# Kernel optimization log

Measured on AMD Instinct MI355X. Metric: run time of the kernel, lower is better.

The kernel has to match this reference:

```python
import jax, jax.numpy as jnp
import numpy as np
from jax import lax

V = 9; C1 = 80; C2 = 40; C4 = 24; CH = 32
H1, W1 = 30, 40; H2, W2 = 60, 80; H4, W4 = 120, 160
SHAPE = (96, 96, 96); N = 131072; EPS = 1e-5
OFFS = np.stack(np.meshgrid(np.arange(-1, 2), np.arange(-1, 2), np.arange(-1, 2), indexing='ij'), -1).reshape(-1, 3).astype(np.int32)  # 27 kernel offsets


def conv2d(x, w, b):
    y = lax.conv_general_dilated(x, w, (1, 1), 'SAME', dimension_numbers=('NCHW', 'OIHW', 'NCHW'))
    return y + b[None, :, None, None]


def bn1d(x, g, b):  # eval-mode BatchNorm1d (running_mean=0, running_var=1)
    return g * x * (1.0 / np.sqrt(1.0 + EPS)) + b


def layernorm(x, g, b):
    m = x.mean(-1, keepdims=True)
    v = ((x - m) ** 2).mean(-1, keepdims=True)
    return (x - m) / jnp.sqrt(v + EPS) * g + b


def grid_sample_zeros(img, gx, gy):
    # img [V,C,H,W]; gx,gy [V,M] normalized to [-1,1]; bilinear, align_corners=True, zeros padding
    Vn, C, H, W = img.shape
    px = (gx + 1.0) * 0.5 * (W - 1)
    py = (gy + 1.0) * 0.5 * (H - 1)
    x0 = jnp.floor(px); y0 = jnp.floor(py)
    wx = px - x0; wy = py - y0
    flat = img.reshape(Vn, C, H * W)
    def corner(xc, yc, wgt):
        valid = (xc >= 0) & (xc <= W - 1) & (yc >= 0) & (yc <= H - 1)
        xi = jnp.clip(xc, 0, W - 1).astype(jnp.int32)
        yi = jnp.clip(yc, 0, H - 1).astype(jnp.int32)
        idx = yi * W + xi  # [V,M]
        g = jax.vmap(lambda f, i: f[:, i])(flat, idx)  # [V,C,M]
        return g * (wgt * valid)[:, None, :]
    return (corner(x0, y0, (1 - wx) * (1 - wy)) + corner(x0 + 1, y0, wx * (1 - wy))
            + corner(x0, y0 + 1, (1 - wx) * wy) + corner(x0 + 1, y0 + 1, wx * wy))


def subm_conv(feat, W3, cxyz, grid):
    # submanifold sparse 3x3x3 conv: per-offset gather of active neighbors -> GEMM -> accumulate
    n = feat.shape[0]
    shp = jnp.asarray(SHAPE, jnp.int32)
    out = jnp.zeros((n, W3.shape[-1]), feat.dtype)
    for k in range(27):
        nc = cxyz + jnp.asarray(OFFS[k])
        inb = jnp.all((nc >= 0) & (nc < shp), axis=1)
        ncc = jnp.clip(nc, 0, shp - 1)
        idx = grid[ncc[:, 0], ncc[:, 1], ncc[:, 2]]
        ok = (inb & (idx >= 0)).astype(feat.dtype)
        g = feat[jnp.clip(idx, 0, n - 1)] * ok[:, None]
        out = out + g @ W3[k]
    return out


def _forward(feats_1x, feats_2x, feats_4x, origin, voxel_size, KRcam,
             w_f1, b_f1, w_f2, b_f2, w_f4, b_f4, w_down, b_down,
             w_p1, b_p1, w_p2, b_p2, w_p3, b_p3, w_p4, b_p4,
             bn0_g, bn0_b, w_elan, w_s1, ln1_g, ln1_b, w_s2, ln2_g, ln2_b,
             w_s3, ln3_g, ln3_b, w_s4, bn4_g, bn4_b,
             coords, stage, min_view_number):
    # feat_fusion_pre (bs=1, take batch 0)
    f1 = jax.nn.relu(conv2d(feats_1x[:, 0], w_f1, b_f1))
    f2 = jax.nn.relu(conv2d(feats_2x[:, 0], w_f2, b_f2))
    f4 = jax.nn.relu(conv2d(feats_4x[:, 0], w_f4, b_f4))
    f1 = jax.image.resize(f1, (V, C1, H2, W2), 'bilinear')  # F.interpolate x2
    f4 = f4.reshape(V, C4, H2, 2, W2, 2).mean(axis=(3, 5))  # AvgPool2d(2)
    fuse = jnp.concatenate([f1, f2, f4], axis=1)
    fuse = jax.nn.relu(conv2d(fuse, w_down, b_down))
    for w, b in ((w_p1, b_p1), (w_p2, b_p2), (w_p3, b_p3), (w_p4, b_p4)):
        fuse = fuse + jax.nn.relu(conv2d(fuse, w, b))  # residual blocks -> [V,CH,H2,W2]
    # multi-view projection
    cxyz = coords[:, 1:]
    world = cxyz.astype(jnp.float32) * voxel_size + origin[0]
    hom = jnp.concatenate([world, jnp.ones_like(world[:, :1])], axis=1)  # [N,4]
    im_p = jnp.einsum('vij,nj->vin', KRcam[:, 0], hom)  # [V,3,N]
    im_z = im_p[:, 2]
    gx = 2.0 * (im_p[:, 0] / im_z) / (W4 - 1) - 1.0
    gy = 2.0 * (im_p[:, 1] / im_z) / (H4 - 1) - 1.0
    mask = (jnp.abs(gx) <= 1) & (jnp.abs(gy) <= 1) & (im_z > 0)  # [V,N]
    count = mask.sum(0).astype(jnp.float32)
    # inputs are constructed so every voxel is seen by all views: valid_voxel compaction == identity
    feats = grid_sample_zeros(fuse, gx, gy) * mask[:, None, :]  # [V,CH,N]
    feat = feats.transpose(2, 0, 1)  # [N,V,CH]
    m = mask.T.astype(feat.dtype)  # [N,V]
    den = m.sum(1, keepdims=True)
    mean = (m[..., None] * feat).sum(1) / den
    var = (m[..., None] * (feat - mean[:, None, :]) ** 2).sum(1) / den  # [N,CH]
    # sparse subm conv chain
    sc = cxyz // (2 ** (2 - stage))  # stage=2 -> identity
    grid = jnp.full(SHAPE, -1, jnp.int32).at[sc[:, 0], sc[:, 1], sc[:, 2]].set(jnp.arange(N, dtype=jnp.int32))
    x = bn1d(var, bn0_g, bn0_b)
    x = jax.nn.relu(subm_conv(x, w_elan, sc, grid))  # Spares3dELAN stand-in
    r = jax.nn.relu(subm_conv(x, w_s1, sc, grid)); x = layernorm(r + x, ln1_g, ln1_b)
    r = jax.nn.relu(subm_conv(x, w_s2, sc, grid)); x = layernorm(r + x, ln2_g, ln2_b)
    r = jax.nn.relu(subm_conv(x, w_s3, sc, grid)); x = layernorm(r + x, ln3_g, ln3_b)
    occ = bn1d(subm_conv(x, w_s4, sc, grid), bn4_g, bn4_b)  # [N,1]
    return occ, coords, count


def setup_inputs() -> dict:
    key = jax.random.key(0)
    keys = jax.random.split(key, 40)
    ki = iter(range(40))
    def rn(shape, s=1.0):
        return jax.random.normal(keys[next(ki)], shape, jnp.float32) * s
    inp = {}
    inp['feats_1x'] = rn((V, 1, C1, H1, W1))
    inp['feats_2x'] = rn((V, 1, C2, H2, W2))
    inp['feats_4x'] = rn((V, 1, C4, H4, W4))
    flat = np.arange(N, dtype=np.int64) * 6  # unique active voxels in a 96^3 grid
    cx = flat // (96 * 96); rem = flat % (96 * 96)
    inp['coords'] = jnp.asarray(np.stack([np.zeros(N, np.int64), cx, rem // 96, rem % 96], 1), jnp.int32)
    inp['origin'] = jnp.asarray([[-1.92, -1.92, 1.0]], jnp.float32)
    inp['voxel_size'] = jnp.float32(0.04)
    fx, fy = 38.0, 28.0
    P = np.zeros((V, 1, 3, 4), np.float32)
    for v in range(V):
        P[v, 0] = np.array([[fx, 0.0, (W4 - 1) / 2, fx * 0.02 * (v - 4)],
                            [0.0, fy, (H4 - 1) / 2, 0.0],
                            [0.0, 0.0, 1.0, 0.0]], np.float32)
    inp['KRcam'] = jnp.asarray(P)
    s = 0.05
    inp['w_f1'] = rn((C1, C1, 3, 3), s); inp['b_f1'] = rn((C1,), s)
    inp['w_f2'] = rn((C2, C2, 3, 3), s); inp['b_f2'] = rn((C2,), s)
    inp['w_f4'] = rn((C4, C4, 3, 3), s); inp['b_f4'] = rn((C4,), s)
    inp['w_down'] = rn((CH, C1 + C2 + C4, 1, 1), s); inp['b_down'] = rn((CH,), s)
    for i in (1, 2, 3, 4):
        inp['w_p%d' % i] = rn((CH, CH, 3, 3), s); inp['b_p%d' % i] = rn((CH,), s)
    inp['bn0_g'] = jnp.ones((CH,), jnp.float32); inp['bn0_b'] = jnp.zeros((CH,), jnp.float32)
    inp['w_elan'] = rn((27, CH, CH), s)
    inp['w_s1'] = rn((27, CH, CH), s); inp['ln1_g'] = jnp.ones((CH,), jnp.float32); inp['ln1_b'] = jnp.zeros((CH,), jnp.float32)
    inp['w_s2'] = rn((27, CH, CH), s); inp['ln2_g'] = jnp.ones((CH,), jnp.float32); inp['ln2_b'] = jnp.zeros((CH,), jnp.float32)
    inp['w_s3'] = rn((27, CH, CH), s); inp['ln3_g'] = jnp.ones((CH,), jnp.float32); inp['ln3_b'] = jnp.zeros((CH,), jnp.float32)
    inp['w_s4'] = rn((27, CH, 1), s); inp['bn4_g'] = jnp.ones((1,), jnp.float32); inp['bn4_b'] = jnp.zeros((1,), jnp.float32)
    inp['stage'] = 2
    inp['min_view_number'] = 1
    return inp


def reference(feats_1x, feats_2x, feats_4x, origin, voxel_size, KRcam,
              w_f1, b_f1, w_f2, b_f2, w_f4, b_f4, w_down, b_down,
              w_p1, b_p1, w_p2, b_p2, w_p3, b_p3, w_p4, b_p4,
              bn0_g, bn0_b, w_elan, w_s1, ln1_g, ln1_b, w_s2, ln2_g, ln2_b,
              w_s3, ln3_g, ln3_b, w_s4, bn4_g, bn4_b,
              coords, stage, min_view_number):
    return _forward(feats_1x, feats_2x, feats_4x, origin, voxel_size, KRcam,
                    w_f1, b_f1, w_f2, b_f2, w_f4, b_f4, w_down, b_down,
                    w_p1, b_p1, w_p2, b_p2, w_p3, b_p3, w_p4, b_p4,
                    bn0_g, bn0_b, w_elan, w_s1, ln1_g, ln1_b, w_s2, ln2_g, ln2_b,
                    w_s3, ln3_g, ln3_b, w_s4, bn4_g, bn4_b,
                    coords, stage, min_view_number)
```

## Files before the change

### kernel.cpp

```cpp
#include <hip/hip_runtime.h>
#include <math.h>

#define VN 9
#define NVOX 131072
#define GS 96
static constexpr float INVS = 0.9999950000374997f;

typedef short bf16x8 __attribute__((ext_vector_type(8)));
typedef float f32x4v __attribute__((ext_vector_type(4)));

__device__ inline float4 ld4(const float* p){ return *reinterpret_cast<const float4*>(p); }

__device__ inline ushort f2b(float f){
  unsigned u = __float_as_uint(f);
  unsigned r = (u + 0x7fffu + ((u >> 16) & 1u)) >> 16;
  return (ushort)r;
}
__device__ inline float b2f(ushort s){ return __uint_as_float(((unsigned)s) << 16); }
__device__ inline float blo(unsigned u){ return __uint_as_float(u << 16); }
__device__ inline float bhi(unsigned u){ return __uint_as_float(u & 0xffff0000u); }

__device__ inline float4 ld4b(const ushort* p){
  uint2 u = *reinterpret_cast<const uint2*>(p);
  float4 r; r.x = blo(u.x); r.y = bhi(u.x); r.z = blo(u.y); r.w = bhi(u.y); return r;
// ... 117 lines not shown
  int wave = tid >> 6;
  int vbase = bid*(MT*64) + wave*(MT*16);
  int m = lane & 15, q = lane >> 4;
  int HW = H*W;
  int p[MT], py[MT], px[MT]; bool pin[MT];
  #pragma unroll
  for (int t = 0; t < MT; ++t){
    int pp = vbase + t*16 + m;
    pin[t] = pp < total;
    if (pp > total-1) pp = total-1;
    p[t] = pp;
    int v = pp / HW; int rem = pp - v*HW;
    int y = rem / W;
    py[t] = y; px[t] = rem - y*W;
  }
  f32x4v acc[MT][NT];
  #pragma unroll
  for (int t = 0; t < MT; ++t)
    #pragma unroll
    for (int n = 0; n < NT; ++n) acc[t][n] = 0.f;
  bf16x8 z = (short)0;

  #pragma unroll 1
  for (int tap = 0; tap < TAPS; ++tap){
    int dy = (TAPS == 9) ? tap/3 - 1 : 0;
    int dx = (TAPS == 9) ? tap%3 - 1 : 0;
    int off = dy*W + dx;
    bool val[MT];
    #pragma unroll
    for (int t = 0; t < MT; ++t)
      val[t] = pin[t] && ((unsigned)(py[t]+dy) < (unsigned)H)
                      && ((unsigned)(px[t]+dx) < (unsigned)W);
    #pragma unroll
    for (int ck = 0; ck < CK; ++ck){
      bf16x8 Af[MT], Bf[NT];
      #pragma unroll
      for (int t = 0; t < MT; ++t){
        size_t idx = val[t] ? (size_t)(p[t]+off) : 0;
        bf16x8 a = *(const bf16x8*)(fin + idx*CIN + ck*32 + q*8);
        Af[t] = val[t] ? a : z;
      }
      #pragma unroll
      for (int n = 0; n < NT; ++n)
        Bf[n] = *(const bf16x8*)(w2 + ((size_t)((tap*CK+ck)*COP + n*16 + m))*32 + q*8);
      #pragma unroll
      for (int t = 0; t < MT; ++t)
        #pragma unroll
        for (int n = 0; n < NT; ++n)
          acc[t][n] = __builtin_amdgcn_mfma_f32_16x16x32_bf16(Bf[n], Af[t], acc[t][n], 0, 0, 0);
    }
  }

  #pragma unroll
  for (int n = 0; n < NT; ++n){
    int co4 = n*16 + q*4;
    bool cok = co4 < Cout;
    float4 bs = cok ? ld4(bias + co4) : float4{0.f,0.f,0.f,0.f};
    #pragma unroll
    for (int t = 0; t < MT; ++t){
      int pp = vbase + t*16 + m;
      if (pp < total && cok){
        float4 v;
        v.x = fmaxf(acc[t][n][0] + bs.x, 0.f);
        v.y = fmaxf(acc[t][n][1] + bs.y, 0.f);
        v.z = fmaxf(acc[t][n][2] + bs.z, 0.f);
        v.w = fmaxf(acc[t][n][3] + bs.w, 0.f);
        st4b(outp + (size_t)pp*outStride + outOff + co4, v);
      }
    }
  }
}

template<int TH, int NT>
__device__ void conv_lds_dev(
    const ushort* __restrict__ fin, const ushort* __restrict__ w2,
    const float* __restrict__ bias, ushort* __restrict__ outp,
    int H, int W, int Cout, int outStride,
    const ushort* __restrict__ skipin, ushort* lds, int bid, int tid){
  constexpr int RPW = TH/4;
  constexpr int PS = 36;
  int xtiles = W >> 4;
  int ytiles = (H + TH - 1) / TH;
  int v  = bid / (ytiles*xtiles);
  int rem = bid - v*(ytiles*xtiles);
  int ty = (rem / xtiles) * TH;
  int tx = (rem % xtiles) * 16;
  const ushort* ibase = fin + (size_t)v*H*W*32;
  for (int i = tid; i < (TH+2)*18*4; i += 256){
    int chunk = i & 3;
    int pxi = i >> 2;
    int ly = pxi / 18, lx = pxi - ly*18;
    int gy = ty + ly - 1, gx = tx + lx - 1;
    uint4 d = {0,0,0,0};
    if ((unsigned)gy < (unsigned)H && (unsigned)gx < (unsigned)W)
      d = *(const uint4*)(ibase + ((size_t)gy*W + gx)*32 + chunk*8);
    *(uint4*)(lds + (size_t)(ly*18 + lx)*PS + chunk*8) = d;
  }
  __syncthreads();
  int lane = tid & 63;
  int wave = tid >> 6;
  int m = lane & 15, q = lane >> 4;
  f32x4v acc[RPW][NT];
  #pragma unroll
  for (int t = 0; t < RPW; ++t)
    #pragma unroll
    for (int n = 0; n < NT; ++n) acc[t][n] = 0.f;

  #pragma unroll 1
  for (int tap = 0; tap < 9; ++tap){
    int dy = tap/3 - 1, dx = tap%3 - 1;
    bf16x8 Af[RPW], Bf[NT];
    #pragma unroll
    for (int t = 0; t < RPW; ++t){
      int ly = wave*RPW + t + 1 + dy;
      int lx = m + 1 + dx;
      Af[t] = *(const bf16x8*)(lds + (size_t)(ly*18 + lx)*PS + q*8);
    }
    #pragma unroll
    for (int n = 0; n < NT; ++n)
      Bf[n] = *(const bf16x8*)(w2 + ((size_t)(tap*(NT*16) + n*16 + m))*32 + q*8);
    #pragma unroll
    for (int t = 0; t < RPW; ++t)
      #pragma unroll
      for (int n = 0; n < NT; ++n)
        acc[t][n] = __builtin_amdgcn_mfma_f32_16x16x32_bf16(Bf[n], Af[t], acc[t][n], 0, 0, 0);
  }

  #pragma unroll
  for (int n = 0; n < NT; ++n){
    int co4 = n*16 + q*4;
    bool cok = co4 < Cout;
    float4 bs = cok ? ld4(bias + co4) : float4{0.f,0.f,0.f,0.f};
    #pragma unroll
    for (int t = 0; t < RPW; ++t){
      int y = ty + wave*RPW + t;
      int x = tx + m;
      if (y < H && cok){
        size_t pp = (size_t)(v*H + y)*W + x;
        float4 val;
        val.x = fmaxf(acc[t][n][0] + bs.x, 0.f);
        val.y = fmaxf(acc[t][n][1] + bs.y, 0.f);
        val.z = fmaxf(acc[t][n][2] + bs.z, 0.f);
        val.w = fmaxf(acc[t][n][3] + bs.w, 0.f);
        if (skipin){
          float4 sk = ld4b(skipin + pp*32 + co4);
          val.x += sk.x; val.y += sk.y; val.z += sk.z; val.w += sk.w;
        }
        st4b(outp + pp*outStride + co4, val);
      }
    }
  }
}

__global__ __launch_bounds__(256) void k_conv_lds4(
    const ushort* __restrict__ fin, const ushort* __restrict__ w2,
    const float* __restrict__ bias, ushort* __restrict__ outp,
    const ushort* __restrict__ skipin){
  __shared__ ushort lds[6*18*36];
  conv_lds_dev<4,2>(fin, w2, bias, outp, 60, 80, 32, 32, skipin, lds, blockIdx.x, threadIdx.x);
}

__global__ __launch_bounds__(256) void k_down_p0(
    const ushort* __restrict__ fcat, const ushort* __restrict__ wdn,
    const float* __restrict__ b_dn, const ushort* __restrict__ wp0,
    const float* __restrict__ b_p0, ushort* __restrict__ outB){
  __shared__ ushort ldsA[6*18*36];
  int bid = blockIdx.x;
  int tid = threadIdx.x;
  int v  = bid / 75;
  int rem = bid - v*75;
  int ty = (rem / 5) * 4;
  int tx = (rem % 5) * 16;
  int lane = tid & 63;
  int wave = tid >> 6;
  int m = lane & 15, q = lane >> 4;
  bf16x8 z = (short)0;

  #pragma unroll
  for (int t = 0; t < 2; ++t){
    int hp = (wave*2 + t)*16 + m;
    int hpc = hp < 108 ? hp : 107;
    int ly = hpc / 18, lx = hpc - ly*18;
    int gy = ty + ly - 1, gx = tx + lx - 1;
    bool ok = (hp < 108) && ((unsigned)gy < 60u) && ((unsigned)gx < 80u);
    size_t pbase = ((size_t)(v*60 + (ok ? gy : 0))*80 + (ok ? gx : 0))*160;
    f32x4v acc0 = 0.f, acc1 = 0.f;
    #pragma unroll
    for (int ck = 0; ck < 5; ++ck){
      bf16x8 a = *(const bf16x8*)(fcat + pbase + ck*32 + q*8);
      if (!ok) a = z;
      bf16x8 w0 = *(const bf16x8*)(wdn + ((size_t)(ck*32 + m))*32 + q*8);
      bf16x8 w1 = *(const bf16x8*)(wdn + ((size_t)(ck*32 + 16 + m))*32 + q*8);
      acc0 = __builtin_amdgcn_mfma_f32_16x16x32_bf16(w0, a, acc0, 0, 0, 0);
      acc1 = __builtin_amdgcn_mfma_f32_16x16x32_bf16(w1, a, acc1, 0, 0, 0);
    }
    if (hp < 108){
      float4 bs0 = ld4(b_dn + q*4);
      float4 bs1 = ld4(b_dn + 16 + q*4);
      float4 v0, v1;
      v0.x = ok ? fmaxf(acc0[0] + bs0.x, 0.f) : 0.f;
      v0.y = ok ? fmaxf(acc0[1] + bs0.y, 0.f) : 0.f;
      v0.z = ok ? fmaxf(acc0[2] + bs0.z, 0.f) : 0.f;
      v0.w = ok ? fmaxf(acc0[3] + bs0.w, 0.f) : 0.f;
      v1.x = ok ? fmaxf(acc1[0] + bs1.x, 0.f) : 0.f;
      v1.y = ok ? fmaxf(acc1[1] + bs1.y, 0.f) : 0.f;
      v1.z = ok ? fmaxf(acc1[2] + bs1.z, 0.f) : 0.f;
      v1.w = ok ? fmaxf(acc1[3] + bs1.w, 0.f) : 0.f;
      st4b(ldsA + (size_t)(ly*18 + lx)*36 + q*4,      v0);
      st4b(ldsA + (size_t)(ly*18 + lx)*36 + 16 + q*4, v1);
    }
  }
  __syncthreads();

  f32x4v pacc0 = 0.f, pacc1 = 0.f;
  #pragma unroll 1
  for (int tap = 0; tap < 9; ++tap){
    int dy = tap/3 - 1, dx = tap%3 - 1;
    bf16x8 Af = *(const bf16x8*)(ldsA + (size_t)((wave+1+dy)*18 + (m+1+dx))*36 + q*8);
    bf16x8 B0 = *(const bf16x8*)(wp0 + ((size_t)(tap*32 + m))*32 + q*8);
    bf16x8 B1 = *(const bf16x8*)(wp0 + ((size_t)(tap*32 + 16 + m))*32 + q*8);
    pacc0 = __builtin_amdgcn_mfma_f32_16x16x32_bf16(B0, Af, pacc0, 0, 0, 0);
    pacc1 = __builtin_amdgcn_mfma_f32_16x16x32_bf16(B1, Af, pacc1, 0, 0, 0);
  }
  int y = ty + wave, x = tx + m;
  size_t pp = (size_t)(v*60 + y)*80 + x;
  #pragma unroll
  for (int n = 0; n < 2; ++n){
    int co4 = n*16 + q*4;
    float4 bs = ld4(b_p0 + co4);
    f32x4v& pa = n ? pacc1 : pacc0;
    float4 sk = ld4b(ldsA + (size_t)((wave+1)*18 + (m+1))*36 + co4);
    float4 val;
    val.x = fmaxf(pa[0] + bs.x, 0.f) + sk.x;
    val.y = fmaxf(pa[1] + bs.y, 0.f) + sk.y;
    val.z = fmaxf(pa[2] + bs.z, 0.f) + sk.z;
    val.w = fmaxf(pa[3] + bs.w, 0.f) + sk.w;
    st4b(outB + pp*32 + co4, val);
  }
}

__global__ __launch_bounds__(256) void k_p2_p3(
    const ushort* __restrict__ finA, const ushort* __restrict__ wp2,
    const float* __restrict__ b_p2, const ushort* __restrict__ wp3,
    const float* __restrict__ b_p3, ushort* __restrict__ outB){
  __shared__ ushort ldsIn[8*20*36];
  __shared__ ushort ldsMid[6*18*36];
  int bid = blockIdx.x;
  int tid = threadIdx.x;
  int v  = bid / 75;
  int rem = bid - v*75;
  int ty = (rem / 5) * 4;
  int tx = (rem % 5) * 16;
  for (int i = tid; i < 8*20*4; i += 256){
    int chunk = i & 3;
    int pxi = i >> 2;
    int ly = pxi / 20, lx = pxi - ly*20;
    int gy = ty + ly - 2, gx = tx + lx - 2;
    uint4 d = {0,0,0,0};
    if ((unsigned)gy < 60u && (unsigned)gx < 80u)
      d = *(const uint4*)(finA + ((size_t)(v*60 + gy)*80 + gx)*32 + chunk*8);
    *(uint4*)(ldsIn + (size_t)(ly*20 + lx)*36 + chunk*8) = d;
  }
  __syncthreads();
  int lane = tid & 63;
  int wave = tid >> 6;
  int m = lane & 15, q = lane >> 4;

  #pragma unroll
  for (int t = 0; t < 2; ++t){
    int hp = (wave*2 + t)*16 + m;
    int hpc = hp < 108 ? hp : 107;
    int ly = hpc / 18, lx = hpc - ly*18;
    int gy = ty + ly - 1, gx = tx + lx - 1;
    bool ok = (hp < 108) && ((unsigned)gy < 60u) && ((unsigned)gx < 80u);
    f32x4v acc0 = 0.f, acc1 = 0.f;
    #pragma unroll 1
    for (int tap = 0; tap < 9; ++tap){
      int dy = tap/3 - 1, dx = tap%3 - 1;
      bf16x8 a = *(const bf16x8*)(ldsIn + (size_t)((ly+dy+1)*20 + (lx+dx+1))*36 + q*8);
      bf16x8 w0 = *(const bf16x8*)(wp2 + ((size_t)(tap*32 + m))*32 + q*8);
      bf16x8 w1 = *(const bf16x8*)(wp2 + ((size_t)(tap*32 + 16 + m))*32 + q*8);
      acc0 = __builtin_amdgcn_mfma_f32_16x16x32_bf16(w0, a, acc0, 0, 0, 0);
      acc1 = __builtin_amdgcn_mfma_f32_16x16x32_bf16(w1, a, acc1, 0, 0, 0);
    }
    if (hp < 108){
      float4 bs0 = ld4(b_p2 + q*4);
      float4 bs1 = ld4(b_p2 + 16 + q*4);
      float4 sk0 = ld4b(ldsIn + (size_t)((ly+1)*20 + (lx+1))*36 + q*4);
      float4 sk1 = ld4b(ldsIn + (size_t)((ly+1)*20 + (lx+1))*36 + 16 + q*4);
      float4 v0, v1;
      v0.x = ok ? fmaxf(acc0[0] + bs0.x, 0.f) + sk0.x : 0.f;
      v0.y = ok ? fmaxf(acc0[1] + bs0.y, 0.f) + sk0.y : 0.f;
      v0.z = ok ? fmaxf(acc0[2] + bs0.z, 0.f) + sk0.z : 0.f;
      v0.w = ok ? fmaxf(acc0[3] + bs0.w, 0.f) + sk0.w : 0.f;
      v1.x = ok ? fmaxf(acc1[0] + bs1.x, 0.f) + sk1.x : 0.f;
      v1.y = ok ? fmaxf(acc1[1] + bs1.y, 0.f) + sk1.y : 0.f;
      v1.z = ok ? fmaxf(acc1[2] + bs1.z, 0.f) + sk1.z : 0.f;
      v1.w = ok ? fmaxf(acc1[3] + bs1.w, 0.f) + sk1.w : 0.f;
      st4b(ldsMid + (size_t)(ly*18 + lx)*36 + q*4,      v0);
      st4b(ldsMid + (size_t)(ly*18 + lx)*36 + 16 + q*4, v1);
    }
  }
  __syncthreads();

  f32x4v pacc0 = 0.f, pacc1 = 0.f;
  #pragma unroll 1
  for (int tap = 0; tap < 9; ++tap){
    int dy = tap/3 - 1, dx = tap%3 - 1;
    bf16x8 a = *(const bf16x8*)(ldsMid + (size_t)((wave+1+dy)*18 + (m+1+dx))*36 + q*8);
    bf16x8 w0 = *(const bf16x8*)(wp3 + ((size_t)(tap*32 + m))*32 + q*8);
    bf16x8 w1 = *(const bf16x8*)(wp3 + ((size_t)(tap*32 + 16 + m))*32 + q*8);
    pacc0 = __builtin_amdgcn_mfma_f32_16x16x32_bf16(w0, a, pacc0, 0, 0, 0);
    pacc1 = __builtin_amdgcn_mfma_f32_16x16x32_bf16(w1, a, pacc1, 0, 0, 0);
  }
  int y = ty + wave, x = tx + m;
  size_t pp = (size_t)(v*60 + y)*80 + x;
  #pragma unroll
  for (int n = 0; n < 2; ++n){
    int co4 = n*16 + q*4;
    float4 bs = ld4(b_p3 + co4);
    f32x4v& pa = n ? pacc1 : pacc0;
    float4 sk = ld4b(ldsMid + (size_t)((wave+1)*18 + (m+1))*36 + co4);
    float4 val;
    val.x = fmaxf(pa[0] + bs.x, 0.f) + sk.x;
    val.y = fmaxf(pa[1] + bs.y, 0.f) + sk.y;
    val.z = fmaxf(pa[2] + bs.z, 0.f) + sk.z;
    val.w = fmaxf(pa[3] + bs.w, 0.f) + sk.w;
    st4b(outB + pp*32 + co4, val);
  }
}

__device__ void scatter_dev(const int* __restrict__ coords, const int* __restrict__ stage,
                            int* __restrict__ grid, int* __restrict__ scn,
                            float* __restrict__ coords_out,
                            const float* __restrict__ origin, const float* __restrict__ vsz,
                            const float* __restrict__ KR,
                            ushort* __restrict__ sidx, float4* __restrict__ swf,
                            float* __restrict__ cnt, int n){
  int c0 = coords[n*4], c1 = coords[n*4+1], c2 = coords[n*4+2], c3 = coords[n*4+3];
  coords_out[n*4+0] = (float)c0;
  coords_out[n*4+1] = (float)c1;
  coords_out[n*4+2] = (float)c2;
  coords_out[n*4+3] = (float)c3;
  int sh = 2 - stage[0];
  int s1 = c1 >> sh, s2 = c2 >> sh, s3 = c3 >> sh;
  scn[n*3+0] = s1; scn[n*3+1] = s2; scn[n*3+2] = s3;
  grid[(s1*GS + s2)*GS + s3] = n;

  float vs = vsz[0];
  float wx = (float)c1*vs + origin[0];
  float wy = (float)c2*vs + origin[1];
  float wz = (float)c3*vs + origin[2];
  float den = 0.f;
  #pragma unroll 1
  for (int v = 0; v < VN; ++v){
    const float* P = KR + v*12;
    float ix = P[0]*wx + P[1]*wy + P[2]*wz + P[3];
    float iy = P[4]*wx + P[5]*wy + P[6]*wz + P[7];
    float iz = P[8]*wx + P[9]*wy + P[10]*wz + P[11];
    float gx = 2.f*(ix/iz)/159.f - 1.f;
    float gy = 2.f*(iy/iz)/119.f - 1.f;
    bool ok = (fabsf(gx) <= 1.f) && (fabsf(gy) <= 1.f) && (iz > 0.f);
    float px = ok ? (gx + 1.f)*0.5f*79.f : 0.f;
    float py = ok ? (gy + 1.f)*0.5f*59.f : 0.f;
    float x0f = floorf(px), y0f = floorf(py);
    float fx = px - x0f, fy = py - y0f;
    int idx = (int)y0f*80 + (int)x0f;
    float mf = ok ? 1.f : 0.f;
    den += mf;
    float4 w;
    w.x = (1.f-fx)*(1.f-fy)*mf;
    w.y = fx*(1.f-fy)*mf;
    w.z = (1.f-fx)*fy*mf;
    w.w = fx*fy*mf;
    sidx[(size_t)v*NVOX + n] = (ushort)idx;
    swf[(size_t)v*NVOX + n] = w;
  }
  cnt[n] = den;
}

__global__ __launch_bounds__(256) void k_heads(
    const ushort* nhwc1, const ushort* wf1, const float* b_f1, ushort* t1,
    const ushort* nhwc2, const ushort* wf2, const float* b_f2, ushort* fcat,
    const ushort* nhwc4, const ushort* wf4, const float* b_f4, ushort* t4,
    const int* coords, const int* stage, int* grid, int* scn, float* coords_out,
    const float* origin, const float* vsz, const float* KR,
    ushort* sidx, float4* swf, float* cnt){
  __shared__ ushort lds[18*18*36];
  int bid = blockIdx.x;
  int tid = threadIdx.x;
  if (bid < 169){ conv_dev<3,5,9,1>(nhwc1, wf1, b_f1, t1, 30, 40, 10800, 80, 80, 0, bid, tid); return; }
  bid -= 169;
  if (bid < 720){ conv_lds_dev<16,2>(nhwc4, wf4, b_f4, t4, 120, 160, 24, 24, nullptr, lds, bid, tid); return; }
  bid -= 720;
  if (bid < 675){ conv_dev<2,3,9,1>(nhwc2, wf2, b_f2, fcat, 60, 80, 43200, 40, 160, 80, bid, tid); return; }
  bid -= 675;
  { int n = bid*256 + tid;
    scatter_dev(coords, stage, grid, scn, coords_out, origin, vsz, KR, sidx, swf, cnt, n); }
}

__global__ __launch_bounds__(256) void k_respool_nbr(
    const ushort* __restrict__ t1, const ushort* __restrict__ t4, ushort* __restrict__ fc,
    const int* __restrict__ scn, const int* __restrict__ grid,
    int* __restrict__ nbr, unsigned* __restrict__ gmask16){
  __shared__ unsigned m16[4];
  int bid = blockIdx.x;
  int tidx = threadIdx.x;
  if (bid < 5063){
    int tid = bid*256 + tidx;
    if (tid < 864000){
      int c4 = tid % 20;
      int x  = (tid / 20) % 80;
      int y  = (tid / 1600) % 60;
      int v  = tid / 96000;
      int c = c4*4;
      int ky = y >> 1; int y0, y1; float wy0, wy1;
      if ((y & 1) == 0){ y0 = ky-1; y1 = ky; wy0 = 0.25f; wy1 = 0.75f; if (y0 < 0){ y0 = 0; wy0 = 0.f; wy1 = 1.f; } }
      else             { y0 = ky; y1 = ky+1; wy0 = 0.75f; wy1 = 0.25f; if (y1 > 29){ y1 = 29; wy1 = 0.f; wy0 = 1.f; } }
      int kx = x >> 1; int x0, x1; float wx0, wx1;
      if ((x & 1) == 0){ x0 = kx-1; x1 = kx; wx0 = 0.25f; wx1 = 0.75f; if (x0 < 0){ x0 = 0; wx0 = 0.f; wx1 = 1.f; } }
      else             { x0 = kx; x1 = kx+1; wx0 = 0.75f; wx1 = 0.25f; if (x1 > 39){ x1 = 39; wx1 = 0.f; wx0 = 1.f; } }
      float4 a00 = ld4b(t1 + ((size_t)(v*30 + y0)*40 + x0)*80 + c);
      float4 a01 = ld4b(t1 + ((size_t)(v*30 + y0)*40 + x1)*80 + c);
      float4 a10 = ld4b(t1 + ((size_t)(v*30 + y1)*40 + x0)*80 + c);
      float4 a11 = ld4b(t1 + ((size_t)(v*30 + y1)*40 + x1)*80 + c);
      float w00 = wy0*wx0, w01 = wy0*wx1, w10 = wy1*wx0, w11 = wy1*wx1;
      float4 r;
      r.x = w00*a00.x + w01*a01.x + w10*a10.x + w11*a11.x;
      r.y = w00*a00.y + w01*a01.y + w10*a10.y + w11*a11.y;
      r.z = w00*a00.z + w01*a01.z + w10*a10.z + w11*a11.z;
      r.w = w00*a00.w + w01*a01.w + w10*a10.w + w11*a11.w;
      st4b(fc + ((size_t)(v*60 + y)*80 + x)*160 + c, r);
      return;
    }
    int t = tid - 864000;
    if (t >= 432000) return;
    int c4 = t % 10;
    int x  = (t / 10) % 80;
    int y  = (t / 800) % 60;
    int v  = t / 48000;
    if (c4 < 6){
      int c = c4*4;
      const ushort* b0 = t4 + ((size_t)(v*120 + 2*y)*160 + 2*x)*24 + c;
      float4 a = ld4b(b0), b = ld4b(b0 + 24), cc = ld4b(b0 + 160*24), d = ld4b(b0 + 160*24 + 24);
      float4 r;
      r.x = 0.25f*(a.x + b.x + cc.x + d.x);
      r.y = 0.25f*(a.y + b.y + cc.y + d.y);
      r.z = 0.25f*(a.z + b.z + cc.z + d.z);
      r.w = 0.25f*(a.w + b.w + cc.w + d.w);
      st4b(fc + ((size_t)(v*60 + y)*80 + x)*160 + 120 + c, r);
    } else {
      float4 zz = {0.f,0.f,0.f,0.f};
      st4b(fc + ((size_t)(v*60 + y)*80 + x)*160 + 144 + (c4-6)*4, zz);
    }
    return;
  }
  bid -= 5063;
  if (tidx < 4) m16[tidx] = 0;
  __syncthreads();
  int vb = bid*64;
  int lane = tidx & 63;
  int wv = tidx >> 6;
  int n = vb + lane;
  int sx = scn[n*3+0], sy = scn[n*3+1], sz = scn[n*3+2];
  int k0 = wv*7;
  int k1 = min(27, k0 + 7);
  unsigned msk = 0;
  #pragma unroll 1
  for (int k = k0; k < k1; ++k){
    int dx = k/9 - 1, dy = (k/3)%3 - 1, dz = k%3 - 1;
    int nx = sx+dx, ny = sy+dy, nz = sz+dz;
    int idx = -1;
    if (((unsigned)nx < 96u) && ((unsigned)ny < 96u) && ((unsigned)nz < 96u))
      idx = grid[(nx*GS + ny)*GS + nz];
    unsigned long long b = __ballot(idx >= 0);
// ... 119 lines not shown
      }
    }
    bf16x8 A0, B0, A1 = zc, B1 = zc, A2 = zc, B2 = zc, t;
    bf16x8 w10 = zc, w11 = zc, w20 = zc, w21 = zc;
    t = *(const bf16x8*)(fin + (size_t)(a0 < 0 ? 0 : a0)*32 + q*8); A0 = (a0 < 0) ? zc : t;
    t = *(const bf16x8*)(fin + (size_t)(b0 < 0 ? 0 : b0)*32 + q*8); B0 = (b0 < 0) ? zc : t;
    bf16x8 w00 = *(const bf16x8*)(w2 + (size_t)(k0*32 + m)*32 + q*8);
    bf16x8 w01 = *(const bf16x8*)(w2 + (size_t)(k0*32 + 16 + m)*32 + q*8);
    if (k1 >= 0){
      t = *(const bf16x8*)(fin + (size_t)(a1 < 0 ? 0 : a1)*32 + q*8); A1 = (a1 < 0) ? zc : t;
      t = *(const bf16x8*)(fin + (size_t)(b1 < 0 ? 0 : b1)*32 + q*8); B1 = (b1 < 0) ? zc : t;
      w10 = *(const bf16x8*)(w2 + (size_t)(k1*32 + m)*32 + q*8);
      w11 = *(const bf16x8*)(w2 + (size_t)(k1*32 + 16 + m)*32 + q*8);
    }
    if (k2 >= 0){
      t = *(const bf16x8*)(fin + (size_t)(a2 < 0 ? 0 : a2)*32 + q*8); A2 = (a2 < 0) ? zc : t;
      t = *(const bf16x8*)(fin + (size_t)(b2 < 0 ? 0 : b2)*32 + q*8); B2 = (b2 < 0) ? zc : t;
      w20 = *(const bf16x8*)(w2 + (size_t)(k2*32 + m)*32 + q*8);
      w21 = *(const bf16x8*)(w2 + (size_t)(k2*32 + 16 + m)*32 + q*8);
    }
    acc[0][0] = __builtin_amdgcn_mfma_f32_16x16x32_bf16(w00, A0, acc[0][0], 0, 0, 0);
    acc[0][1] = __builtin_amdgcn_mfma_f32_16x16x32_bf16(w01, A0, acc[0][1], 0, 0, 0);
    acc[1][0] = __builtin_amdgcn_mfma_f32_16x16x32_bf16(w00, B0, acc[1][0], 0, 0, 0);
    acc[1][1] = __builtin_amdgcn_mfma_f32_16x16x32_bf16(w01, B0, acc[1][1], 0, 0, 0);
    if (k1 >= 0){
      acc[0][0] = __builtin_amdgcn_mfma_f32_16x16x32_bf16(w10, A1, acc[0][0], 0, 0, 0);
      acc[0][1] = __builtin_amdgcn_mfma_f32_16x16x32_bf16(w11, A1, acc[0][1], 0, 0, 0);
      acc[1][0] = __builtin_amdgcn_mfma_f32_16x16x32_bf16(w10, B1, acc[1][0], 0, 0, 0);
      acc[1][1] = __builtin_amdgcn_mfma_f32_16x16x32_bf16(w11, B1, acc[1][1], 0, 0, 0);
    }
    if (k2 >= 0){
      acc[0][0] = __builtin_amdgcn_mfma_f32_16x16x32_bf16(w20, A2, acc[0][0], 0, 0, 0);
      acc[0][1] = __builtin_amdgcn_mfma_f32_16x16x32_bf16(w21, A2, acc[0][1], 0, 0, 0);
      acc[1][0] = __builtin_amdgcn_mfma_f32_16x16x32_bf16(w20, B2, acc[1][0], 0, 0, 0);
      acc[1][1] = __builtin_amdgcn_mfma_f32_16x16x32_bf16(w21, B2, acc[1][1], 0, 0, 0);
    }
  }

  float4 g0v{0,0,0,0}, g1v{0,0,0,0}, b0v{0,0,0,0}, b1v{0,0,0,0};
  if (MODE == 1){
    g0v = ld4(lng + q*4);  g1v = ld4(lng + 16 + q*4);
    b0v = ld4(lnb + q*4);  b1v = ld4(lnb + 16 + q*4);
  }
  #pragma unroll
  for (int t = 0; t < 2; ++t){
    int vox = vb + t*16 + m;
    float x0[4], x1[4];
    #pragma unroll
    for (int r = 0; r < 4; ++r){
      x0[r] = fmaxf(acc[t][0][r], 0.f);
      x1[r] = fmaxf(acc[t][1][r], 0.f);
    }
    if (MODE == 1){
      uint2 sk0 = *(const uint2*)(fin + (size_t)vox*32 + q*4);
      uint2 sk1 = *(const uint2*)(fin + (size_t)vox*32 + 16 + q*4);
      x0[0] += blo(sk0.x); x0[1] += bhi(sk0.x); x0[2] += blo(sk0.y); x0[3] += bhi(sk0.y);
      x1[0] += blo(sk1.x); x1[1] += bhi(sk1.x); x1[2] += blo(sk1.y); x1[3] += bhi(sk1.y);
      float s = (x0[0]+x0[1]+x0[2]+x0[3]) + (x1[0]+x1[1]+x1[2]+x1[3]);
      s += __shfl_xor(s, 16);
      s += __shfl_xor(s, 32);
      float mean = s * (1.f/32.f);
      float v2 = 0.f;
      #pragma unroll
      for (int r = 0; r < 4; ++r){
        x0[r] -= mean; x1[r] -= mean;
        v2 += x0[r]*x0[r] + x1[r]*x1[r];
      }
      v2 += __shfl_xor(v2, 16);
      v2 += __shfl_xor(v2, 32);
      float rs = 1.f / sqrtf(v2*(1.f/32.f) + 1e-5f);
      x0[0] = x0[0]*rs*g0v.x + b0v.x; x0[1] = x0[1]*rs*g0v.y + b0v.y;
      x0[2] = x0[2]*rs*g0v.z + b0v.z; x0[3] = x0[3]*rs*g0v.w + b0v.w;
      x1[0] = x1[0]*rs*g1v.x + b1v.x; x1[1] = x1[1]*rs*g1v.y + b1v.y;
      x1[2] = x1[2]*rs*g1v.z + b1v.z; x1[3] = x1[3]*rs*g1v.w + b1v.w;
    }
    st4b(fout + (size_t)vox*32 + q*4,      float4{x0[0],x0[1],x0[2],x0[3]});
    st4b(fout + (size_t)vox*32 + 16 + q*4, float4{x1[0],x1[1],x1[2],x1[3]});
  }
}

__global__ __launch_bounds__(256) void k_s4(
    const ushort* __restrict__ fin, const float* __restrict__ w4,
    const int* __restrict__ nbr, const unsigned* __restrict__ gmask16,
    const float* __restrict__ bn4g, const float* __restrict__ bn4b,
    float* __restrict__ occ){
  int tid = blockIdx.x*256 + threadIdx.x;
  int n = tid >> 2;
  int part = tid & 3;
  unsigned rem = gmask16[n >> 4];
  float acc = 0.f;
  while (rem){
    int k0 = __ffs(rem) - 1; rem &= rem - 1;
    int k1 = -1;
    if (rem){ k1 = __ffs(rem) - 1; rem &= rem - 1; }
    int i0 = nbr[(size_t)k0*NVOX + n];
    int i1 = (k1 >= 0) ? nbr[(size_t)k1*NVOX + n] : -1;
    uint4 d0 = *(const uint4*)(fin + (size_t)(i0 < 0 ? 0 : i0)*32 + part*8);
    uint4 d1 = {0,0,0,0};
    if (k1 >= 0) d1 = *(const uint4*)(fin + (size_t)(i1 < 0 ? 0 : i1)*32 + part*8);
    if (i0 >= 0){
      float4 wa = ld4(w4 + k0*32 + part*8);
      float4 wb = ld4(w4 + k0*32 + part*8 + 4);
      acc += blo(d0.x)*wa.x + bhi(d0.x)*wa.y + blo(d0.y)*wa.z + bhi(d0.y)*wa.w
           + blo(d0.z)*wb.x + bhi(d0.z)*wb.y + blo(d0.w)*wb.z + bhi(d0.w)*wb.w;
    }
    if (i1 >= 0){
      float4 wa = ld4(w4 + k1*32 + part*8);
      float4 wb = ld4(w4 + k1*32 + part*8 + 4);
      acc += blo(d1.x)*wa.x + bhi(d1.x)*wa.y + blo(d1.y)*wa.z + bhi(d1.y)*wa.w
           + blo(d1.z)*wb.x + bhi(d1.z)*wb.y + blo(d1.w)*wb.z + bhi(d1.w)*wb.w;
    }
  }
  acc += __shfl_xor(acc, 1, 4);
  acc += __shfl_xor(acc, 2, 4);
  if (part == 0) occ[n] = bn4g[0]*acc*INVS + bn4b[0];
}

extern "C" void kernel_launch(void* const* d_in, const int* in_sizes, int n_in,
                              void* d_out, int out_size, void* d_ws, size_t ws_size,
                              hipStream_t stream){
  const float* feats1 = (const float*)d_in[0];
  const float* feats2 = (const float*)d_in[1];
  const float* feats4 = (const float*)d_in[2];
  const int*   coords = (const int*)d_in[3];
  const float* origin = (const float*)d_in[4];
  const float* vsz    = (const float*)d_in[5];
  const float* KR     = (const float*)d_in[6];
  const float* w_f1 = (const float*)d_in[7];  const float* b_f1 = (const float*)d_in[8];
  const float* w_f2 = (const float*)d_in[9];  const float* b_f2 = (const float*)d_in[10];
  const float* w_f4 = (const float*)d_in[11]; const float* b_f4 = (const float*)d_in[12];
  const float* w_dn = (const float*)d_in[13]; const float* b_dn = (const float*)d_in[14];
  const float* w_p[4] = {(const float*)d_in[15], (const float*)d_in[17],
                         (const float*)d_in[19], (const float*)d_in[21]};
  const float* b_p[4] = {(const float*)d_in[16], (const float*)d_in[18],
                         (const float*)d_in[20], (const float*)d_in[22]};
  const float* bn0g = (const float*)d_in[23]; const float* bn0b = (const float*)d_in[24];
  const float* w_elan = (const float*)d_in[25];
  const float* w_s1 = (const float*)d_in[26]; const float* ln1g = (const float*)d_in[27]; const float* ln1b = (const float*)d_in[28];
  const float* w_s2 = (const float*)d_in[29]; const float* ln2g = (const float*)d_in[30]; const float* ln2b = (const float*)d_in[31];
  const float* w_s3 = (const float*)d_in[32]; const float* ln3g = (const float*)d_in[33]; const float* ln3b = (const float*)d_in[34];
  const float* w_s4 = (const float*)d_in[35]; const float* bn4g = (const float*)d_in[36]; const float* bn4b = (const float*)d_in[37];
  const int* stage  = (const int*)d_in[38];
  float* out = (float*)d_out;
  char* base = (char*)d_ws;

  size_t off = 0;
  auto alloc = [&](size_t bytes)->char*{ char* p = base + off; off += (bytes + 255) & ~(size_t)255; return p; };
  ushort* nhwc1 = (ushort*)alloc((size_t)9*30*40*96*2);
  ushort* nhwc2 = (ushort*)alloc((size_t)9*60*80*64*2);
  ushort* nhwc4 = (ushort*)alloc((size_t)9*120*160*32*2);
  ushort* t1    = (ushort*)alloc((size_t)9*30*40*80*2);
  ushort* t4    = (ushort*)alloc((size_t)9*120*160*24*2);
  ushort* fcat  = (ushort*)alloc((size_t)9*60*80*160*2);
  ushort* A     = (ushort*)alloc((size_t)9*60*80*32*2);
  ushort* B     = (ushort*)alloc((size_t)9*60*80*32*2);
  ushort* Fb0   = (ushort*)alloc((size_t)NVOX*32*2);
  ushort* Fb1   = (ushort*)alloc((size_t)NVOX*32*2);
  int*    nbr   = (int*)alloc((size_t)27*NVOX*4);
  int*    grid  = (int*)alloc((size_t)GS*GS*GS*4);
  int*    scn   = (int*)alloc((size_t)NVOX*3*4);
  unsigned* gmask16 = (unsigned*)alloc((size_t)(NVOX/16)*4);
  ushort* wf1   = (ushort*)alloc(9*3*80*32*2);
  ushort* wf2   = (ushort*)alloc(9*2*48*32*2);
  ushort* wf4   = (ushort*)alloc(9*1*32*32*2);
  ushort* wdn   = (ushort*)alloc(1*5*32*32*2);
  ushort* wp0   = (ushort*)alloc(9*1*32*32*2);
  ushort* wp1   = (ushort*)alloc(9*1*32*32*2);
  ushort* wp2   = (ushort*)alloc(9*1*32*32*2);
  ushort* wp3   = (ushort*)alloc(9*1*32*32*2);
  ushort* w2e   = (ushort*)alloc(27*1024*2);
  ushort* w2s1  = (ushort*)alloc(27*1024*2);
  ushort* w2s2  = (ushort*)alloc(27*1024*2);
  ushort* w2s3  = (ushort*)alloc(27*1024*2);
  ushort* sidx  = (ushort*)alloc((size_t)VN*NVOX*2);
  float4* swf   = (float4*)alloc((size_t)VN*NVOX*16);

  k_prep<<<8012,256,0,stream>>>(
      w_f1, w_f2, w_f4, w_dn, w_p[0], w_p[1], w_p[2], w_p[3],
      w_elan, w_s1, w_s2, w_s3,
      wf1, wf2, wf4, wdn, wp0, wp1, wp2, wp3, w2e, w2s1, w2s2, w2s3, grid,
      feats1, feats2, feats4, nhwc1, nhwc2, nhwc4);

  k_heads<<<169 + 720 + 675 + 512,256,0,stream>>>(
      nhwc1, wf1, b_f1, t1,
      nhwc2, wf2, b_f2, fcat,
      nhwc4, wf4, b_f4, t4,
      coords, stage, grid, scn, out + NVOX,
      origin, vsz, KR, sidx, swf, out + 5*NVOX);

  k_respool_nbr<<<5063 + 2048,256,0,stream>>>(t1, t4, fcat, scn, grid, nbr, gmask16);

  k_down_p0<<<675,256,0,stream>>>(fcat, wdn, b_dn, wp0, b_p[0], B);
  k_conv_lds4<<<675,256,0,stream>>>(B, wp1, b_p[1], A, B);
  k_p2_p3<<<675,256,0,stream>>>(A, wp2, b_p[2], wp3, b_p[3], B);

  k_sample<<<NVOX/32,256,0,stream>>>(B, sidx, swf, out + 5*NVOX, bn0g, bn0b, Fb0);

  k_subm_mfma<0><<<NVOX/128,256,0,stream>>>(Fb0, w2e,  nbr, gmask16, nullptr, nullptr, Fb1);
  k_subm_mfma<1><<<NVOX/128,256,0,stream>>>(Fb1, w2s1, nbr, gmask16, ln1g, ln1b, Fb0);
  k_subm_mfma<1><<<NVOX/128,256,0,stream>>>(Fb0, w2s2, nbr, gmask16, ln2g, ln2b, Fb1);
  k_subm_mfma<1><<<NVOX/128,256,0,stream>>>(Fb1, w2s3, nbr, gmask16, ln3g, ln3b, Fb0);

  k_s4<<<NVOX/64,256,0,stream>>>(Fb0, w_s4, nbr, gmask16, bn4g, bn4b, out);
}
```

Before: 330.1 us.

## Fuse downsample and four post-convs into one halo-recompute LDS kernel

Merges the 1x1 downsample conv, p0, p1, p2 and p3 3x3 convs into a single kernel per 4x16 tile, keeping intermediates in two ping-pong LDS buffers with a 4-pixel halo that shrinks each stage. This removes two kernel launches and the global round trips of the intermediate A/B feature maps. In exchange it recomputes halo pixels (the first stage covers 288 positions for 64 outputs) and uses more LDS per block, which may reduce occupancy.

```diff
diff --git a/kernel.cpp b/kernel.cpp
--- a/kernel.cpp
+++ b/kernel.cpp
@@ -293,19 +293,16 @@
   }
 }
 
-__global__ __launch_bounds__(256) void k_conv_lds4(
-    const ushort* __restrict__ fin, const ushort* __restrict__ w2,
-    const float* __restrict__ bias, ushort* __restrict__ outp,
-    const ushort* __restrict__ skipin){
-  __shared__ ushort lds[6*18*36];
-  conv_lds_dev<4,2>(fin, w2, bias, outp, 60, 80, 32, 32, skipin, lds, blockIdx.x, threadIdx.x);
-}
-
-__global__ __launch_bounds__(256) void k_down_p0(
+__global__ __launch_bounds__(256) void k_pchain(
     const ushort* __restrict__ fcat, const ushort* __restrict__ wdn,
-    const float* __restrict__ b_dn, const ushort* __restrict__ wp0,
-    const float* __restrict__ b_p0, ushort* __restrict__ outB){
-  __shared__ ushort ldsA[6*18*36];
+    const float* __restrict__ b_dn,
+    const ushort* __restrict__ wp0, const float* __restrict__ b_p0,
+    const ushort* __restrict__ wp1, const float* __restrict__ b_p1,
+    const ushort* __restrict__ wp2, const float* __restrict__ b_p2,
+    const ushort* __restrict__ wp3, const float* __restrict__ b_p3,
+    ushort* __restrict__ outB){
+  __shared__ ushort bufA[12*24*36];
+  __shared__ ushort bufB[10*22*36];
   int bid = blockIdx.x;
   int tid = threadIdx.x;
   int v  = bid / 75;
@@ -317,13 +314,13 @@
   int m = lane & 15, q = lane >> 4;
   bf16x8 z = (short)0;
 
-  #pragma unroll
-  for (int t = 0; t < 2; ++t){
-    int hp = (wave*2 + t)*16 + m;
-    int hpc = hp < 108 ? hp : 107;
-    int ly = hpc / 18, lx = hpc - ly*18;
-    int gy = ty + ly - 1, gx = tx + lx - 1;
-    bool ok = (hp < 108) && ((unsigned)gy < 60u) && ((unsigned)gx < 80u);
+  #pragma unroll 1
+  for (int t = 0; t < 5; ++t){
+    int hp = (t*4 + wave)*16 + m;
+    int hpc = hp < 288 ? hp : 287;
+    int ly = hpc / 24, lx = hpc - ly*24;
+    int gy = ty + ly - 4, gx = tx + lx - 4;
+    bool ok = (hp < 288) && ((unsigned)gy < 60u) && ((unsigned)gx < 80u);
     size_t pbase = ((size_t)(v*60 + (ok ? gy : 0))*80 + (ok ? gx : 0))*160;
     f32x4v acc0 = 0.f, acc1 = 0.f;
     #pragma unroll
@@ -335,7 +332,7 @@
       acc0 = __builtin_amdgcn_mfma_f32_16x16x32_bf16(w0, a, acc0, 0, 0, 0);
       acc1 = __builtin_amdgcn_mfma_f32_16x16x32_bf16(w1, a, acc1, 0, 0, 0);
     }
-    if (hp < 108){
+    if (hp < 288){
       float4 bs0 = ld4(b_dn + q*4);
       float4 bs1 = ld4(b_dn + 16 + q*4);
       float4 v0, v1;
@@ -347,88 +344,34 @@
       v1.y = ok ? fmaxf(acc1[1] + bs1.y, 0.f) : 0.f;
       v1.z = ok ? fmaxf(acc1[2] + bs1.z, 0.f) : 0.f;
       v1.w = ok ? fmaxf(acc1[3] + bs1.w, 0.f) : 0.f;
-      st4b(ldsA + (size_t)(ly*18 + lx)*36 + q*4,      v0);
-      st4b(ldsA + (size_t)(ly*18 + lx)*36 + 16 + q*4, v1);
+      st4b(bufA + (size_t)(ly*24 + lx)*36 + q*4,      v0);
+      st4b(bufA + (size_t)(ly*24 + lx)*36 + 16 + q*4, v1);
     }
   }
   __syncthreads();
 
-  f32x4v pacc0 = 0.f, pacc1 = 0.f;
   #pragma unroll 1
-  for (int tap = 0; tap < 9; ++tap){
-    int dy = tap/3 - 1, dx = tap%3 - 1;
-    bf16x8 Af = *(const bf16x8*)(ldsA + (size_t)((wave+1+dy)*18 + (m+1+dx))*36 + q*8);
-    bf16x8 B0 = *(const bf16x8*)(wp0 + ((size_t)(tap*32 + m))*32 + q*8);
-    bf16x8 B1 = *(const bf16x8*)(wp0 + ((size_t)(tap*32 + 16 + m))*32 + q*8);
-    pacc0 = __builtin_amdgcn_mfma_f32_16x16x32_bf16(B0, Af, pacc0, 0, 0, 0);
-    pacc1 = __builtin_amdgcn_mfma_f32_16x16x32_bf16(B1, Af, pacc1, 0, 0, 0);
-  }
-  int y = ty + wave, x = tx + m;
-  size_t pp = (size_t)(v*60 + y)*80 + x;
-  #pragma unroll
-  for (int n = 0; n < 2; ++n){
-    int co4 = n*16 + q*4;
-    float4 bs = ld4(b_p0 + co4);
-    f32x4v& pa = n ? pacc1 : pacc0;
-    float4 sk = ld4b(ldsA + (size_t)((wave+1)*18 + (m+1))*36 + co4);
-    float4 val;
-    val.x = fmaxf(pa[0] + bs.x, 0.f) + sk.x;
-    val.y = fmaxf(pa[1] + bs.y, 0.f) + sk.y;
-    val.z = fmaxf(pa[2] + bs.z, 0.f) + sk.z;
-    val.w = fmaxf(pa[3] + bs.w, 0.f) + sk.w;
-    st4b(outB + pp*32 + co4, val);
-  }
-}
-
-__global__ __launch_bounds__(256) void k_p2_p3(
-    const ushort* __restrict__ finA, const ushort* __restrict__ wp2,
-    const float* __restrict__ b_p2, const ushort* __restrict__ wp3,
-    const float* __restrict__ b_p3, ushort* __restrict__ outB){
-  __shared__ ushort ldsIn[8*20*36];
-  __shared__ ushort ldsMid[6*18*36];
-  int bid = blockIdx.x;
-  int tid = threadIdx.x;
-  int v  = bid / 75;
-  int rem = bid - v*75;
-  int ty = (rem / 5) * 4;
-  int tx = (rem % 5) * 16;
-  for (int i = tid; i < 8*20*4; i += 256){
-    int chunk = i & 3;
-    int pxi = i >> 2;
-    int ly = pxi / 20, lx = pxi - ly*20;
-    int gy = ty + ly - 2, gx = tx + lx - 2;
-    uint4 d = {0,0,0,0};
-    if ((unsigned)gy < 60u && (unsigned)gx < 80u)
-      d = *(const uint4*)(finA + ((size_t)(v*60 + gy)*80 + gx)*32 + chunk*8);
-    *(uint4*)(ldsIn + (size_t)(ly*20 + lx)*36 + chunk*8) = d;
-  }
-  __syncthreads();
-  int lane = tid & 63;
-  int wave = tid >> 6;
-  int m = lane & 15, q = lane >> 4;
-
-  #pragma unroll
-  for (int t = 0; t < 2; ++t){
-    int hp = (wave*2 + t)*16 + m;
-    int hpc = hp < 108 ? hp : 107;
-    int ly = hpc / 18, lx = hpc - ly*18;
-    int gy = ty + ly - 1, gx = tx + lx - 1;
-    bool ok = (hp < 108) && ((unsigned)gy < 60u) && ((unsigned)gx < 80u);
+  for (int t = 0; t < 4; ++t){
+    int hp = (t*4 + wave)*16 + m;
+    int hpc = hp < 220 ? hp : 219;
+    int ly = hpc / 22, lx = hpc - ly*22;
+    int gy = ty + ly - 3, gx = tx + lx - 3;
+    bool ok = (hp < 220) && ((unsigned)gy < 60u) && ((unsigned)gx < 80u);
     f32x4v acc0 = 0.f, acc1 = 0.f;
     #pragma unroll 1
     for (int tap = 0; tap < 9; ++tap){
       int dy = tap/3 - 1, dx = tap%3 - 1;
-      bf16x8 a = *(const bf16x8*)(ldsIn + (size_t)((ly+dy+1)*20 + (lx+dx+1))*36 + q*8);
-      bf16x8 w0 = *(const bf16x8*)(wp2 + ((size_t)(tap*32 + m))*32 + q*8);
-      bf16x8 w1 = *(const bf16x8*)(wp2 + ((size_t)(tap*32 + 16 + m))*32 + q*8);
+      bf16x8 a = *(const bf16x8*)(bufA + (size_t)((ly+1+dy)*24 + (lx+1+dx))*36 + q*8);
+      bf16x8 w0 = *(const bf16x8*)(wp0 + ((size_t)(tap*32 + m))*32 + q*8);
+      bf16x8 w1 = *(const bf16x8*)(wp0 + ((size_t)(tap*32 + 16 + m))*32 + q*8);
       acc0 = __builtin_amdgcn_mfma_f32_16x16x32_bf16(w0, a, acc0, 0, 0, 0);
       acc1 = __builtin_amdgcn_mfma_f32_16x16x32_bf16(w1, a, acc1, 0, 0, 0);
     }
-    if (hp < 108){
-      float4 bs0 = ld4(b_p2 + q*4);
-      float4 bs1 = ld4(b_p2 + 16 + q*4);
-      float4 sk0 = ld4b(ldsIn + (size_t)((ly+1)*20 + (lx+1))*36 + q*4);
-      float4 sk1 = ld4b(ldsIn + (size_t)((ly+1)*20 + (lx+1))*36 + 16 + q*4);
+    if (hp < 220){
+      float4 bs0 = ld4(b_p0 + q*4);
+      float4 bs1 = ld4(b_p0 + 16 + q*4);
+      float4 sk0 = ld4b(bufA + (size_t)((ly+1)*24 + (lx+1))*36 + q*4);
+      float4 sk1 = ld4b(bufA + (size_t)((ly+1)*24 + (lx+1))*36 + 16 + q*4);
       float4 v0, v1;
       v0.x = ok ? fmaxf(acc0[0] + bs0.x, 0.f) + sk0.x : 0.f;
       v0.y = ok ? fmaxf(acc0[1] + bs0.y, 0.f) + sk0.y : 0.f;
@@ -438,8 +381,82 @@
       v1.y = ok ? fmaxf(acc1[1] + bs1.y, 0.f) + sk1.y : 0.f;
       v1.z = ok ? fmaxf(acc1[2] + bs1.z, 0.f) + sk1.z : 0.f;
       v1.w = ok ? fmaxf(acc1[3] + bs1.w, 0.f) + sk1.w : 0.f;
-      st4b(ldsMid + (size_t)(ly*18 + lx)*36 + q*4,      v0);
-      st4b(ldsMid + (size_t)(ly*18 + lx)*36 + 16 + q*4, v1);
+      st4b(bufB + (size_t)(ly*22 + lx)*36 + q*4,      v0);
+      st4b(bufB + (size_t)(ly*22 + lx)*36 + 16 + q*4, v1);
+    }
+  }
+  __syncthreads();
+
+  #pragma unroll 1
+  for (int t = 0; t < 3; ++t){
+    int hp = (t*4 + wave)*16 + m;
+    int hpc = hp < 160 ? hp : 159;
+    int ly = hpc / 20, lx = hpc - ly*20;
+    int gy = ty + ly - 2, gx = tx + lx - 2;
+    bool ok = (hp < 160) && ((unsigned)gy < 60u) && ((unsigned)gx < 80u);
+    f32x4v acc0 = 0.f, acc1 = 0.f;
+    #pragma unroll 1
+    for (int tap = 0; tap < 9; ++tap){
+      int dy = tap/3 - 1, dx = tap%3 - 1;
+      bf16x8 a = *(const bf16x8*)(bufB + (size_t)((ly+1+dy)*22 + (lx+1+dx))*36 + q*8);
+      bf16x8 w0 = *(const bf16x8*)(wp1 + ((size_t)(tap*32 + m))*32 + q*8);
+      bf16x8 w1 = *(const bf16x8*)(wp1 + ((size_t)(tap*32 + 16 + m))*32 + q*8);
+      acc0 = __builtin_amdgcn_mfma_f32_16x16x32_bf16(w0, a, acc0, 0, 0, 0);
+      acc1 = __builtin_amdgcn_mfma_f32_16x16x32_bf16(w1, a, acc1, 0, 0, 0);
+    }
+    if (hp < 160){
+      float4 bs0 = ld4(b_p1 + q*4);
+      float4 bs1 = ld4(b_p1 + 16 + q*4);
+      float4 sk0 = ld4b(bufB + (size_t)((ly+1)*22 + (lx+1))*36 + q*4);
+      float4 sk1 = ld4b(bufB + (size_t)((ly+1)*22 + (lx+1))*36 + 16 + q*4);
+      float4 v0, v1;
+      v0.x = ok ? fmaxf(acc0[0] + bs0.x, 0.f) + sk0.x : 0.f;
+      v0.y = ok ? fmaxf(acc0[1] + bs0.y, 0.f) + sk0.y : 0.f;
+      v0.z = ok ? fmaxf(acc0[2] + bs0.z, 0.f) + sk0.z : 0.f;
+      v0.w = ok ? fmaxf(acc0[3] + bs0.w, 0.f) + sk0.w : 0.f;
+      v1.x = ok ? fmaxf(acc1[0] + bs1.x, 0.f) + sk1.x : 0.f;
+      v1.y = ok ? fmaxf(acc1[1] + bs1.y, 0.f) + sk1.y : 0.f;
+      v1.z = ok ? fmaxf(acc1[2] + bs1.z, 0.f) + sk1.z : 0.f;
+      v1.w = ok ? fmaxf(acc1[3] + bs1.w, 0.f) + sk1.w : 0.f;
+      st4b(bufA + (size_t)(ly*20 + lx)*36 + q*4,      v0);
+      st4b(bufA + (size_t)(ly*20 + lx)*36 + 16 + q*4, v1);
+    }
+  }
+  __syncthreads();
+
+  #pragma unroll 1
+  for (int t = 0; t < 2; ++t){
+    int hp = (t*4 + wave)*16 + m;
+    int hpc = hp < 108 ? hp : 107;
+    int ly = hpc / 18, lx = hpc - ly*18;
+    int gy = ty + ly - 1, gx = tx + lx - 1;
+    bool ok = (hp < 108) && ((unsigned)gy < 60u) && ((unsigned)gx < 80u);
+    f32x4v acc0 = 0.f, acc1 = 0.f;
+    #pragma unroll 1
+    for (int tap = 0; tap < 9; ++tap){
+      int dy = tap/3 - 1, dx = tap%3 - 1;
+      bf16x8 a = *(const bf16x8*)(bufA + (size_t)((ly+1+dy)*20 + (lx+1+dx))*36 + q*8);
+      bf16x8 w0 = *(const bf16x8*)(wp2 + ((size_t)(tap*32 + m))*32 + q*8);
+      bf16x8 w1 = *(const bf16x8*)(wp2 + ((size_t)(tap*32 + 16 + m))*32 + q*8);
+      acc0 = __builtin_amdgcn_mfma_f32_16x16x32_bf16(w0, a, acc0, 0, 0, 0);
+      acc1 = __builtin_amdgcn_mfma_f32_16x16x32_bf16(w1, a, acc1, 0, 0, 0);
+    }
+    if (hp < 108){
+      float4 bs0 = ld4(b_p2 + q*4);
+      float4 bs1 = ld4(b_p2 + 16 + q*4);
+      float4 sk0 = ld4b(bufA + (size_t)((ly+1)*20 + (lx+1))*36 + q*4);
+      float4 sk1 = ld4b(bufA + (size_t)((ly+1)*20 + (lx+1))*36 + 16 + q*4);
+      float4 v0, v1;
+      v0.x = ok ? fmaxf(acc0[0] + bs0.x, 0.f) + sk0.x : 0.f;
+      v0.y = ok ? fmaxf(acc0[1] + bs0.y, 0.f) + sk0.y : 0.f;
+      v0.z = ok ? fmaxf(acc0[2] + bs0.z, 0.f) + sk0.z : 0.f;
+      v0.w = ok ? fmaxf(acc0[3] + bs0.w, 0.f) + sk0.w : 0.f;
+      v1.x = ok ? fmaxf(acc1[0] + bs1.x, 0.f) + sk1.x : 0.f;
+      v1.y = ok ? fmaxf(acc1[1] + bs1.y, 0.f) + sk1.y : 0.f;
+      v1.z = ok ? fmaxf(acc1[2] + bs1.z, 0.f) + sk1.z : 0.f;
+      v1.w = ok ? fmaxf(acc1[3] + bs1.w, 0.f) + sk1.w : 0.f;
+      st4b(bufB + (size_t)(ly*18 + lx)*36 + q*4,      v0);
+      st4b(bufB + (size_t)(ly*18 + lx)*36 + 16 + q*4, v1);
     }
   }
   __syncthreads();
@@ -448,7 +465,7 @@
   #pragma unroll 1
   for (int tap = 0; tap < 9; ++tap){
     int dy = tap/3 - 1, dx = tap%3 - 1;
-    bf16x8 a = *(const bf16x8*)(ldsMid + (size_t)((wave+1+dy)*18 + (m+1+dx))*36 + q*8);
+    bf16x8 a = *(const bf16x8*)(bufB + (size_t)((wave+1+dy)*18 + (m+1+dx))*36 + q*8);
     bf16x8 w0 = *(const bf16x8*)(wp3 + ((size_t)(tap*32 + m))*32 + q*8);
     bf16x8 w1 = *(const bf16x8*)(wp3 + ((size_t)(tap*32 + 16 + m))*32 + q*8);
     pacc0 = __builtin_amdgcn_mfma_f32_16x16x32_bf16(w0, a, pacc0, 0, 0, 0);
@@ -461,7 +478,7 @@
     int co4 = n*16 + q*4;
     float4 bs = ld4(b_p3 + co4);
     f32x4v& pa = n ? pacc1 : pacc0;
-    float4 sk = ld4b(ldsMid + (size_t)((wave+1)*18 + (m+1))*36 + co4);
+    float4 sk = ld4b(bufB + (size_t)((wave+1)*18 + (m+1))*36 + co4);
     float4 val;
     val.x = fmaxf(pa[0] + bs.x, 0.f) + sk.x;
     val.y = fmaxf(pa[1] + bs.y, 0.f) + sk.y;
@@ -887,7 +904,6 @@
   ushort* t1    = (ushort*)alloc((size_t)9*30*40*80*2);
   ushort* t4    = (ushort*)alloc((size_t)9*120*160*24*2);
   ushort* fcat  = (ushort*)alloc((size_t)9*60*80*160*2);
-  ushort* A     = (ushort*)alloc((size_t)9*60*80*32*2);
   ushort* B     = (ushort*)alloc((size_t)9*60*80*32*2);
   ushort* Fb0   = (ushort*)alloc((size_t)NVOX*32*2);
   ushort* Fb1   = (ushort*)alloc((size_t)NVOX*32*2);
@@ -925,9 +941,8 @@
 
   k_respool_nbr<<<5063 + 2048,256,0,stream>>>(t1, t4, fcat, scn, grid, nbr, gmask16);
 
-  k_down_p0<<<675,256,0,stream>>>(fcat, wdn, b_dn, wp0, b_p[0], B);
-  k_conv_lds4<<<675,256,0,stream>>>(B, wp1, b_p[1], A, B);
-  k_p2_p3<<<675,256,0,stream>>>(A, wp2, b_p[2], wp3, b_p[3], B);
+  k_pchain<<<675,256,0,stream>>>(fcat, wdn, b_dn, wp0, b_p[0], wp1, b_p[1],
+                                 wp2, b_p[2], wp3, b_p[3], B);
 
   k_sample<<<NVOX/32,256,0,stream>>>(B, sidx, swf, out + 5*NVOX, bn0g, bn0b, Fb0);
 
```

Result: slower. 346.6 us (+5.0%).
